# Kernel optimization log

Hardware: AMD Instinct MI355X
Metric: run time of the kernel (lower is better)

## Reference

```python
import jax, jax.numpy as jnp
import numpy as np

EPS = 1e-06


def setup_inputs() -> dict:
    key = jax.random.key(0)
    k1, k2, k3 = jax.random.split(key, 3)
    B, N, E, Din, U = 8, 1024, 16384, 128, 128
    x = jax.random.normal(k1, (B, N, Din), dtype=jnp.float32)
    node_mask = jnp.ones((B, N), dtype=bool)
    edge_index = jax.random.randint(k2, (B, 2, E), 0, N).astype(jnp.int32)
    edge_mask = jnp.ones((B, E), dtype=bool)
    kernel = jax.random.normal(k3, (Din, U), dtype=jnp.float32) * (1.0 / np.sqrt(Din))
    bias = jnp.zeros((U,), dtype=jnp.float32)
    return {"x": x, "node_mask": node_mask, "edge_index": edge_index,
            "edge_mask": edge_mask, "kernel": kernel, "bias": bias}


def reference(x, node_mask, edge_index, edge_mask, kernel, bias):
    B, N, _ = x.shape
    dtype = x.dtype
    node_mask_f = node_mask.astype(dtype)          # [B, N]
    edge_mask_f = edge_mask.astype(dtype)          # [B, E]
    src = jnp.clip(edge_index[:, 0, :], 0, N - 1)  # [B, E]
    dst = jnp.clip(edge_index[:, 1, :], 0, N - 1)  # [B, E]
    # adjacency[b, n, m] = sum over edges e with dst=n, src=m of edge_mask
    # (identical to the one-hot einsum in the original, built by scatter-add)
    b_idx = jnp.broadcast_to(jnp.arange(B)[:, None], src.shape)
    adjacency = jnp.zeros((B, N, N), dtype=dtype).at[b_idx, dst, src].add(edge_mask_f)
    # masked self-loops
    adjacency = adjacency + node_mask_f[:, :, None] * jnp.eye(N, dtype=dtype)[None]
    degree = jnp.sum(adjacency, axis=-1)           # [B, N]
    inv_sqrt_deg = jax.lax.rsqrt(jnp.maximum(degree, EPS))
    norm_adj = adjacency * inv_sqrt_deg[:, :, None] * inv_sqrt_deg[:, None, :]
    support = jnp.matmul(x, kernel)                # [B, N, U]
    out = jnp.matmul(norm_adj, support) + bias     # [B, N, U]
    return out * node_mask_f[:, :, None]
```

## Files before the change

### kernel.cpp

```cpp
#include <hip/hip_runtime.h>

#define B_   8
#define N_   1024
#define E_   16384
#define DIN_ 128
#define U_   128
#define CAP_ 64

__global__ __launch_bounds__(256) void k_support(
    const float* __restrict__ x, const float* __restrict__ kern,
    float* __restrict__ support, int* __restrict__ counts) {
    const int tid = threadIdx.x;
    const int u = tid & 127;
    const int h = tid >> 7;
    const int bb = blockIdx.x & 7;
    const int rc = blockIdx.x >> 3;
    const int row0 = bb * N_ + rc * 16;
    if (tid < 16) counts[row0 + tid] = 0;
    __shared__ float xs[16][DIN_];
    const float4* xsrc = (const float4*)(x + (size_t)row0 * DIN_);
    #pragma unroll
    for (int i = 0; i < 2; ++i)
        ((float4*)xs)[i * 256 + tid] = xsrc[i * 256 + tid];
    __syncthreads();
    float acc[8] = {0.f,0.f,0.f,0.f,0.f,0.f,0.f,0.f};
    #pragma unroll 4
    for (int d = 0; d < DIN_; ++d) {
        float k = kern[d * U_ + u];
        #pragma unroll
        for (int r = 0; r < 8; ++r) acc[r] = fmaf(xs[h*8+r][d], k, acc[r]);
    }
    #pragma unroll
    for (int r = 0; r < 8; ++r)
        support[(size_t)(row0 + h*8 + r) * U_ + u] = acc[r];
}

__global__ __launch_bounds__(256) void k_fill(
    const int* __restrict__ edge_index, const int* __restrict__ edge_mask,
    int* __restrict__ counts, unsigned short* __restrict__ bucket) {
    const int b     = blockIdx.x & 7;
    const int chunk = blockIdx.x >> 3;
    const int e     = chunk * 256 + threadIdx.x;
    if (edge_mask[(size_t)b * E_ + e] != 0) {
        const int* p = edge_index + (size_t)b * 2 * E_;
        int src = min(max(p[e], 0), N_ - 1);
        int dst = min(max(p[E_ + e], 0), N_ - 1);
        int bn = b * N_ + dst;
        int pos = atomicAdd(&counts[bn], 1);
        if (pos < CAP_) bucket[(size_t)bn * CAP_ + pos] = (unsigned short)src;
    }
}

__global__ __launch_bounds__(256) void k_agg(
    const float* __restrict__ support, const int* __restrict__ node_mask,
    const int* __restrict__ counts, const unsigned short* __restrict__ bucket,
    const float* __restrict__ bias, float* __restrict__ out) {
    const int bi  = blockIdx.x;
    const int swz = (bi & 7) * 512 + (bi >> 3);
    const int h   = threadIdx.x >> 7;
    const int u   = threadIdx.x & 127;
    const int bn  = swz * 2 + h;
    const int b   = bn >> 10;

    __shared__ int2 sp[2][CAP_];

    int nm = node_mask[bn];
    int cnt_true = counts[bn];
    int cnt = min(cnt_true, CAP_);
    float isd_n = rsqrtf(fmaxf((float)cnt_true + (nm ? 1.0f : 0.0f), 1e-6f));
    const unsigned short* bk = bucket + (size_t)bn * CAP_;

    if (u < cnt) {
        int m  = bk[u];
        int gm = b * N_ + m;
        float w = rsqrtf(fmaxf((float)counts[gm] + (node_mask[gm] ? 1.0f : 0.0f), 1e-6f));
        sp[h][u] = make_int2(gm, __float_as_int(w));
    }
    __syncthreads();

    float bs = bias[u];
    float acc = nm ? isd_n * support[(size_t)bn * U_ + u] : 0.f;
    #pragma unroll 4
    for (int t = 0; t < cnt; ++t) {
        int2 p = sp[h][t];
        acc = fmaf(__int_as_float(p.y), support[(size_t)p.x * U_ + u], acc);
    }
    out[(size_t)bn * U_ + u] = nm ? fmaf(isd_n, acc, bs) : 0.f;
}

extern "C" void kernel_launch(void* const* d_in, const int* in_sizes, int n_in,
                              void* d_out, int out_size, void* d_ws, size_t ws_size,
                              hipStream_t stream) {
    const float* x         = (const float*)d_in[0];
    const int*   node_mask = (const int*)d_in[1];
    const int*   edge_index= (const int*)d_in[2];
    const int*   edge_mask = (const int*)d_in[3];
    const float* kern      = (const float*)d_in[4];
    const float* bias      = (const float*)d_in[5];
    float*       out       = (float*)d_out;

    char* ws = (char*)d_ws;
    size_t off = 0;
    float*          support = (float*)(ws + off);          off += (size_t)B_ * N_ * U_ * sizeof(float);
    int*            counts  = (int*)(ws + off);            off += (size_t)B_ * N_ * sizeof(int);
    unsigned short* bucket  = (unsigned short*)(ws + off); off += (size_t)B_ * N_ * CAP_ * sizeof(unsigned short);

    k_support<<<B_ * N_ / 16, 256, 0, stream>>>(x, kern, support, counts);
    k_fill<<<B_ * E_ / 256, 256, 0, stream>>>(edge_index, edge_mask, counts, bucket);
    k_agg<<<B_ * N_ / 2, 256, 0, stream>>>(support, node_mask, counts, bucket, bias, out);
}
```

Baseline: 29.04 us.

## Reorder to aggregate x first then apply GEMM in fused kernel

Uses associativity, (A·X)·W instead of A·(X·W), to aggregate neighbor rows of x directly and then multiply by the weight matrix inside the same kernel. This removes the separate support kernel and the support buffer's write and read-back through global memory. A small kernel now zeroes the counts. The cost is that the GEMM is folded into the aggregation blocks, which carry a shared-memory tile of 8 rows and have fewer blocks (1024 instead of 4096), which may lower occupancy.

```diff
diff --git a/kernel.cpp b/kernel.cpp
--- a/kernel.cpp
+++ b/kernel.cpp
@@ -6,33 +6,10 @@
 #define DIN_ 128
 #define U_   128
 #define CAP_ 64
+#define NPB_ 8
 
-__global__ __launch_bounds__(256) void k_support(
-    const float* __restrict__ x, const float* __restrict__ kern,
-    float* __restrict__ support, int* __restrict__ counts) {
-    const int tid = threadIdx.x;
-    const int u = tid & 127;
-    const int h = tid >> 7;
-    const int bb = blockIdx.x & 7;
-    const int rc = blockIdx.x >> 3;
-    const int row0 = bb * N_ + rc * 16;
-    if (tid < 16) counts[row0 + tid] = 0;
-    __shared__ float xs[16][DIN_];
-    const float4* xsrc = (const float4*)(x + (size_t)row0 * DIN_);
-    #pragma unroll
-    for (int i = 0; i < 2; ++i)
-        ((float4*)xs)[i * 256 + tid] = xsrc[i * 256 + tid];
-    __syncthreads();
-    float acc[8] = {0.f,0.f,0.f,0.f,0.f,0.f,0.f,0.f};
-    #pragma unroll 4
-    for (int d = 0; d < DIN_; ++d) {
-        float k = kern[d * U_ + u];
-        #pragma unroll
-        for (int r = 0; r < 8; ++r) acc[r] = fmaf(xs[h*8+r][d], k, acc[r]);
-    }
-    #pragma unroll
-    for (int r = 0; r < 8; ++r)
-        support[(size_t)(row0 + h*8 + r) * U_ + u] = acc[r];
+__global__ __launch_bounds__(256) void k_zero(int* __restrict__ counts) {
+    counts[blockIdx.x * 256 + threadIdx.x] = 0;
 }
 
 __global__ __launch_bounds__(256) void k_fill(
@@ -51,41 +28,74 @@
     }
 }
 
-__global__ __launch_bounds__(256) void k_agg(
-    const float* __restrict__ support, const int* __restrict__ node_mask,
+__global__ __launch_bounds__(256) void k_agggemm(
+    const float* __restrict__ x, const int* __restrict__ node_mask,
     const int* __restrict__ counts, const unsigned short* __restrict__ bucket,
-    const float* __restrict__ bias, float* __restrict__ out) {
-    const int bi  = blockIdx.x;
-    const int swz = (bi & 7) * 512 + (bi >> 3);
-    const int h   = threadIdx.x >> 7;
-    const int u   = threadIdx.x & 127;
-    const int bn  = swz * 2 + h;
-    const int b   = bn >> 10;
+    const float* __restrict__ kern, const float* __restrict__ bias,
+    float* __restrict__ out) {
+    const int tid   = threadIdx.x;
+    const int b     = blockIdx.x & 7;
+    const int chunk = blockIdx.x >> 3;
+    const int row0  = b * N_ + chunk * NPB_;
 
-    __shared__ int2 sp[2][CAP_];
+    __shared__ float xagg[NPB_][DIN_];
+    __shared__ int2  sp[NPB_][CAP_];
+    __shared__ int   scnt[NPB_];
+    __shared__ float sisd[NPB_];
+    __shared__ int   snm[NPB_];
 
-    int nm = node_mask[bn];
-    int cnt_true = counts[bn];
-    int cnt = min(cnt_true, CAP_);
-    float isd_n = rsqrtf(fmaxf((float)cnt_true + (nm ? 1.0f : 0.0f), 1e-6f));
-    const unsigned short* bk = bucket + (size_t)bn * CAP_;
-
-    if (u < cnt) {
-        int m  = bk[u];
-        int gm = b * N_ + m;
-        float w = rsqrtf(fmaxf((float)counts[gm] + (node_mask[gm] ? 1.0f : 0.0f), 1e-6f));
-        sp[h][u] = make_int2(gm, __float_as_int(w));
+    if (tid < NPB_) {
+        int bn = row0 + tid;
+        int nm = node_mask[bn];
+        int ct = counts[bn];
+        snm[tid]  = nm;
+        scnt[tid] = min(ct, CAP_);
+        sisd[tid] = rsqrtf(fmaxf((float)ct + (nm ? 1.0f : 0.0f), 1e-6f));
     }
     __syncthreads();
 
+    for (int s = tid; s < NPB_ * CAP_; s += 256) {
+        int i = s >> 6, slot = s & (CAP_ - 1);
+        if (slot < scnt[i]) {
+            int m  = bucket[(size_t)(row0 + i) * CAP_ + slot];
+            int gm = b * N_ + m;
+            float w = rsqrtf(fmaxf((float)counts[gm] + (node_mask[gm] ? 1.0f : 0.0f), 1e-6f));
+            sp[i][slot] = make_int2(gm, __float_as_int(w));
+        }
+    }
+    __syncthreads();
+
+    const int u = tid & 127;
+    const int h = tid >> 7;
+    for (int r = 0; r < NPB_ / 2; ++r) {
+        int i   = r * 2 + h;
+        int bn  = row0 + i;
+        int cnt = scnt[i];
+        float isd_n = sisd[i];
+        float acc = snm[i] ? isd_n * x[(size_t)bn * DIN_ + u] : 0.f;
+        #pragma unroll 4
+        for (int t = 0; t < cnt; ++t) {
+            int2 p = sp[i][t];
+            acc = fmaf(__int_as_float(p.y), x[(size_t)p.x * DIN_ + u], acc);
+        }
+        xagg[i][u] = isd_n * acc;
+    }
+    __syncthreads();
+
+    float acc[4] = {0.f, 0.f, 0.f, 0.f};
+    #pragma unroll 4
+    for (int d = 0; d < DIN_; ++d) {
+        float k = kern[d * U_ + u];
+        #pragma unroll
+        for (int r2 = 0; r2 < 4; ++r2)
+            acc[r2] = fmaf(xagg[h * 4 + r2][d], k, acc[r2]);
+    }
     float bs = bias[u];
-    float acc = nm ? isd_n * support[(size_t)bn * U_ + u] : 0.f;
-    #pragma unroll 4
-    for (int t = 0; t < cnt; ++t) {
-        int2 p = sp[h][t];
-        acc = fmaf(__int_as_float(p.y), support[(size_t)p.x * U_ + u], acc);
+    #pragma unroll
+    for (int r2 = 0; r2 < 4; ++r2) {
+        int i = h * 4 + r2;
+        out[(size_t)(row0 + i) * U_ + u] = snm[i] ? (acc[r2] + bs) : 0.f;
     }
-    out[(size_t)bn * U_ + u] = nm ? fmaf(isd_n, acc, bs) : 0.f;
 }
 
 extern "C" void kernel_launch(void* const* d_in, const int* in_sizes, int n_in,
@@ -101,11 +111,11 @@
 
     char* ws = (char*)d_ws;
     size_t off = 0;
-    float*          support = (float*)(ws + off);          off += (size_t)B_ * N_ * U_ * sizeof(float);
     int*            counts  = (int*)(ws + off);            off += (size_t)B_ * N_ * sizeof(int);
     unsigned short* bucket  = (unsigned short*)(ws + off); off += (size_t)B_ * N_ * CAP_ * sizeof(unsigned short);
 
-    k_support<<<B_ * N_ / 16, 256, 0, stream>>>(x, kern, support, counts);
+    k_zero<<<B_ * N_ / 256, 256, 0, stream>>>(counts);
     k_fill<<<B_ * E_ / 256, 256, 0, stream>>>(edge_index, edge_mask, counts, bucket);
-    k_agg<<<B_ * N_ / 2, 256, 0, stream>>>(support, node_mask, counts, bucket, bias, out);
+    k_agggemm<<<B_ * N_ / NPB_, 256, 0, stream>>>(x, node_mask, counts, bucket,
+                                                  kern, bias, out);
 }
```

New measurement: 32.25 us. 1.11x slower.

## Co-schedule support GEMM and edge fill in one launch, wave-per-node aggregation

Applied to the files above, without the earlier changes.

Splits the zeroing of counts into a tiny kernel, then merges the support matmul and the edge bucket fill into one launch whose blocks branch by block index, so the two independent stages can overlap on the GPU. The aggregation kernel now gives each 64-lane wave one node, with float2 loads and neighbor indices and weights broadcast by shuffles instead of through shared memory and a barrier. The added zero kernel brings in an extra launch, and divergent block roles may unbalance the merged kernel.

```diff
diff --git a/kernel.cpp b/kernel.cpp
--- a/kernel.cpp
+++ b/kernel.cpp
@@ -7,47 +7,53 @@
 #define U_   128
 #define CAP_ 64
 
-__global__ __launch_bounds__(256) void k_support(
-    const float* __restrict__ x, const float* __restrict__ kern,
-    float* __restrict__ support, int* __restrict__ counts) {
-    const int tid = threadIdx.x;
-    const int u = tid & 127;
-    const int h = tid >> 7;
-    const int bb = blockIdx.x & 7;
-    const int rc = blockIdx.x >> 3;
-    const int row0 = bb * N_ + rc * 16;
-    if (tid < 16) counts[row0 + tid] = 0;
-    __shared__ float xs[16][DIN_];
-    const float4* xsrc = (const float4*)(x + (size_t)row0 * DIN_);
-    #pragma unroll
-    for (int i = 0; i < 2; ++i)
-        ((float4*)xs)[i * 256 + tid] = xsrc[i * 256 + tid];
-    __syncthreads();
-    float acc[8] = {0.f,0.f,0.f,0.f,0.f,0.f,0.f,0.f};
-    #pragma unroll 4
-    for (int d = 0; d < DIN_; ++d) {
-        float k = kern[d * U_ + u];
-        #pragma unroll
-        for (int r = 0; r < 8; ++r) acc[r] = fmaf(xs[h*8+r][d], k, acc[r]);
-    }
-    #pragma unroll
-    for (int r = 0; r < 8; ++r)
-        support[(size_t)(row0 + h*8 + r) * U_ + u] = acc[r];
+__global__ __launch_bounds__(256) void k_zero(int* __restrict__ counts) {
+    counts[blockIdx.x * 256 + threadIdx.x] = 0;
 }
 
-__global__ __launch_bounds__(256) void k_fill(
+__global__ __launch_bounds__(256) void k_mix(
+    const float* __restrict__ x, const float* __restrict__ kern,
+    float* __restrict__ support,
     const int* __restrict__ edge_index, const int* __restrict__ edge_mask,
     int* __restrict__ counts, unsigned short* __restrict__ bucket) {
-    const int b     = blockIdx.x & 7;
-    const int chunk = blockIdx.x >> 3;
-    const int e     = chunk * 256 + threadIdx.x;
-    if (edge_mask[(size_t)b * E_ + e] != 0) {
-        const int* p = edge_index + (size_t)b * 2 * E_;
-        int src = min(max(p[e], 0), N_ - 1);
-        int dst = min(max(p[E_ + e], 0), N_ - 1);
-        int bn = b * N_ + dst;
-        int pos = atomicAdd(&counts[bn], 1);
-        if (pos < CAP_) bucket[(size_t)bn * CAP_ + pos] = (unsigned short)src;
+    __shared__ float xs[16][DIN_];
+    const int tid = threadIdx.x;
+
+    if (blockIdx.x < 512) {
+        const int bid = blockIdx.x;
+        const int u = tid & 127;
+        const int h = tid >> 7;
+        const int bb = bid & 7;
+        const int rc = bid >> 3;
+        const int row0 = bb * N_ + rc * 16;
+        const float4* xsrc = (const float4*)(x + (size_t)row0 * DIN_);
+        #pragma unroll
+        for (int i = 0; i < 2; ++i)
+            ((float4*)xs)[i * 256 + tid] = xsrc[i * 256 + tid];
+        __syncthreads();
+        float acc[8] = {0.f,0.f,0.f,0.f,0.f,0.f,0.f,0.f};
+        #pragma unroll 4
+        for (int d = 0; d < DIN_; ++d) {
+            float k = kern[d * U_ + u];
+            #pragma unroll
+            for (int r = 0; r < 8; ++r) acc[r] = fmaf(xs[h*8+r][d], k, acc[r]);
+        }
+        #pragma unroll
+        for (int r = 0; r < 8; ++r)
+            support[(size_t)(row0 + h*8 + r) * U_ + u] = acc[r];
+    } else {
+        const int bid   = blockIdx.x - 512;
+        const int b     = bid & 7;
+        const int chunk = bid >> 3;
+        const int e     = chunk * 256 + tid;
+        if (edge_mask[(size_t)b * E_ + e] != 0) {
+            const int* p = edge_index + (size_t)b * 2 * E_;
+            int src = min(max(p[e], 0), N_ - 1);
+            int dst = min(max(p[E_ + e], 0), N_ - 1);
+            int bn = b * N_ + dst;
+            int pos = atomicAdd(&counts[bn], 1);
+            if (pos < CAP_) bucket[(size_t)bn * CAP_ + pos] = (unsigned short)src;
+        }
     }
 }
 
@@ -55,37 +61,43 @@
     const float* __restrict__ support, const int* __restrict__ node_mask,
     const int* __restrict__ counts, const unsigned short* __restrict__ bucket,
     const float* __restrict__ bias, float* __restrict__ out) {
-    const int bi  = blockIdx.x;
-    const int swz = (bi & 7) * 512 + (bi >> 3);
-    const int h   = threadIdx.x >> 7;
-    const int u   = threadIdx.x & 127;
-    const int bn  = swz * 2 + h;
-    const int b   = bn >> 10;
-
-    __shared__ int2 sp[2][CAP_];
+    const int bi   = blockIdx.x;
+    const int lane = threadIdx.x & 63;
+    const int wid  = threadIdx.x >> 6;
+    const int bn   = (bi & 7) * N_ + (bi >> 3) * 4 + wid;
+    const int b    = bn >> 10;
 
     int nm = node_mask[bn];
     int cnt_true = counts[bn];
     int cnt = min(cnt_true, CAP_);
     float isd_n = rsqrtf(fmaxf((float)cnt_true + (nm ? 1.0f : 0.0f), 1e-6f));
-    const unsigned short* bk = bucket + (size_t)bn * CAP_;
 
-    if (u < cnt) {
-        int m  = bk[u];
-        int gm = b * N_ + m;
-        float w = rsqrtf(fmaxf((float)counts[gm] + (node_mask[gm] ? 1.0f : 0.0f), 1e-6f));
-        sp[h][u] = make_int2(gm, __float_as_int(w));
+    int gm = 0; float w = 0.f;
+    if (lane < cnt) {
+        int m = bucket[(size_t)bn * CAP_ + lane];
+        gm = b * N_ + m;
+        w  = rsqrtf(fmaxf((float)counts[gm] + (node_mask[gm] ? 1.0f : 0.0f), 1e-6f));
     }
-    __syncthreads();
 
-    float bs = bias[u];
-    float acc = nm ? isd_n * support[(size_t)bn * U_ + u] : 0.f;
+    const float2* supp2 = (const float2*)support;
+    float2 acc = make_float2(0.f, 0.f);
+    if (nm) {
+        float2 s = supp2[(size_t)bn * 64 + lane];
+        acc.x = isd_n * s.x; acc.y = isd_n * s.y;
+    }
     #pragma unroll 4
     for (int t = 0; t < cnt; ++t) {
-        int2 p = sp[h][t];
-        acc = fmaf(__int_as_float(p.y), support[(size_t)p.x * U_ + u], acc);
+        int   mt = __shfl(gm, t, 64);
+        float wt = __shfl(w,  t, 64);
+        float2 s = supp2[(size_t)mt * 64 + lane];
+        acc.x = fmaf(wt, s.x, acc.x);
+        acc.y = fmaf(wt, s.y, acc.y);
     }
-    out[(size_t)bn * U_ + u] = nm ? fmaf(isd_n, acc, bs) : 0.f;
+    float2 bs = ((const float2*)bias)[lane];
+    float2 o;
+    o.x = nm ? fmaf(isd_n, acc.x, bs.x) : 0.f;
+    o.y = nm ? fmaf(isd_n, acc.y, bs.y) : 0.f;
+    ((float2*)out)[(size_t)bn * 64 + lane] = o;
 }
 
 extern "C" void kernel_launch(void* const* d_in, const int* in_sizes, int n_in,
@@ -105,7 +117,8 @@
     int*            counts  = (int*)(ws + off);            off += (size_t)B_ * N_ * sizeof(int);
     unsigned short* bucket  = (unsigned short*)(ws + off); off += (size_t)B_ * N_ * CAP_ * sizeof(unsigned short);
 
-    k_support<<<B_ * N_ / 16, 256, 0, stream>>>(x, kern, support, counts);
-    k_fill<<<B_ * E_ / 256, 256, 0, stream>>>(edge_index, edge_mask, counts, bucket);
-    k_agg<<<B_ * N_ / 2, 256, 0, stream>>>(support, node_mask, counts, bucket, bias, out);
+    k_zero<<<B_ * N_ / 256, 256, 0, stream>>>(counts);
+    k_mix<<<1024, 256, 0, stream>>>(x, kern, support, edge_index, edge_mask,
+                                    counts, bucket);
+    k_agg<<<B_ * N_ / 4, 256, 0, stream>>>(support, node_mask, counts, bucket, bias, out);
 }
```

Result: slower. 32.51 us (+12.0%).
